# Performance work log

Measured on AMD Instinct MI355X. Metric: run time of the kernel, lower is better.

Reference implementation:

```python
import jax, jax.numpy as jnp
import numpy as np

B, S, D, H = 2, 2048, 2048, 16
HD = D // H
DFF = 4 * D
EPS = 1e-5


def _gelu(x):
    # tanh-approximate GELU as in the torch module
    c = jnp.sqrt(jnp.asarray(2.0 / jnp.pi, dtype=x.dtype))
    return 0.5 * x * (1.0 + jnp.tanh(c * (x + 0.044715 * x ** 3)))


def _layernorm(x, scale, shift):
    mean = jnp.mean(x, axis=-1, keepdims=True)
    var = jnp.mean((x - mean) ** 2, axis=-1, keepdims=True)  # unbiased=False
    return scale * (x - mean) / jnp.sqrt(var + EPS) + shift


def setup_inputs() -> dict:
    key = jax.random.key(0)
    ks = jax.random.split(key, 8)
    std = 0.02
    return {
        "x": jax.random.normal(ks[0], (B, S, D), dtype=jnp.float32),
        "Wq": std * jax.random.normal(ks[1], (D, D), dtype=jnp.float32),
        "Wk": std * jax.random.normal(ks[2], (D, D), dtype=jnp.float32),
        "Wv": std * jax.random.normal(ks[3], (D, D), dtype=jnp.float32),
        "Wo": std * jax.random.normal(ks[4], (D, D), dtype=jnp.float32),
        "bo": jnp.zeros((D,), dtype=jnp.float32),
        "ln1_scale": jnp.ones((D,), dtype=jnp.float32),
        "ln1_shift": jnp.zeros((D,), dtype=jnp.float32),
        "ln2_scale": jnp.ones((D,), dtype=jnp.float32),
        "ln2_shift": jnp.zeros((D,), dtype=jnp.float32),
        "W1": std * jax.random.normal(ks[5], (D, DFF), dtype=jnp.float32),
        "b1": jnp.zeros((DFF,), dtype=jnp.float32),
        "W2": std * jax.random.normal(ks[6], (DFF, D), dtype=jnp.float32),
        "b2": jnp.zeros((D,), dtype=jnp.float32),
    }


def _attention(x, Wq, Wk, Wv, Wo, bo):
    b, s, d = x.shape
    q = (x @ Wq).reshape(b, s, H, HD).transpose(0, 2, 1, 3)  # bhsd
    k = (x @ Wk).reshape(b, s, H, HD).transpose(0, 2, 1, 3)
    v = (x @ Wv).reshape(b, s, H, HD).transpose(0, 2, 1, 3)
    scores = jnp.einsum("bhqd,bhkd->bhqk", q, k)
    causal = jnp.tril(jnp.ones((s, s), dtype=bool))
    scores = jnp.where(causal, scores, -jnp.inf)
    w = jax.nn.softmax(scores / jnp.sqrt(jnp.asarray(HD, dtype=x.dtype)), axis=-1)
    ctx = jnp.einsum("bhqk,bhkd->bhqd", w, v)
    ctx = ctx.transpose(0, 2, 1, 3).reshape(b, s, d)
    return ctx @ Wo + bo


def reference(x, Wq, Wk, Wv, Wo, bo, ln1_scale, ln1_shift, ln2_scale, ln2_shift, W1, b1, W2, b2):
    # pre-LN transformer block; dropout rate 0 -> identity
    h = x + _attention(_layernorm(x, ln1_scale, ln1_shift), Wq, Wk, Wv, Wo, bo)
    y = _gelu(_layernorm(h, ln2_scale, ln2_shift) @ W1 + b1)
    return h + (y @ W2 + b2)
```

## Files before the change

### kernel.cpp

```cpp
#include <hip/hip_runtime.h>
#include <cmath>


typedef unsigned short u16;
typedef unsigned int   u32;
typedef float  f32x4   __attribute__((ext_vector_type(4)));
typedef short  s16x8   __attribute__((ext_vector_type(8)));
typedef short  s16x4   __attribute__((ext_vector_type(4)));
typedef __bf16 bf16x8  __attribute__((ext_vector_type(8)));

#define DEV __device__ __forceinline__

DEV u16 f2bf(float f) {
  union { float f; u32 u; } v; v.f = f;
  u32 u = v.u;
  u += 0x7fffu + ((u >> 16) & 1u);
  return (u16)(u >> 16);
}

DEV f32x4 mfma16(s16x8 a, s16x8 b, f32x4 c) {
  return __builtin_amdgcn_mfma_f32_16x16x32_bf16(
      __builtin_bit_cast(bf16x8, a), __builtin_bit_cast(bf16x8, b), c, 0, 0, 0);
}

DEV float gelu_f(float x) {
  const float c = 0.7978845608028654f;
  const float z = c * (x + 0.044715f * x * x * x);
  const float e = __expf(2.0f * z);
  const float th = 1.0f - 2.0f / (e + 1.0f);
  return 0.5f * x * (1.0f + th);
}

DEV void gload16(const u16* g, u16* l) {
  __builtin_amdgcn_global_load_lds(
      (const __attribute__((address_space(1))) u32*)(const void*)g,
      (__attribute__((address_space(3))) u32*)(void*)l, 16, 0, 0);
}

__global__ __launch_bounds__(256) void transpose_cast(
    const float* __restrict__ W, u16* __restrict__ Wt, int K, int N) {
  __shared__ float tile[32][33];
  const int n0 = blockIdx.x * 32, k0 = blockIdx.y * 32;
  const int tx = threadIdx.x, ty = threadIdx.y;
#pragma unroll
  for (int i = 0; i < 4; ++i)
    tile[ty + 8 * i][tx] = W[(size_t)(k0 + ty + 8 * i) * N + n0 + tx];
  __syncthreads();
#pragma unroll
  for (int i = 0; i < 4; ++i)
    Wt[(size_t)(n0 + ty + 8 * i) * K + k0 + tx] = f2bf(tile[tx][ty + 8 * i]);
}

__global__ __launch_bounds__(256) void transpose_v(
    const u16* __restrict__ QKV, u16* __restrict__ VT) {
  __shared__ u16 tile[32][33];
  const int s0 = blockIdx.x * 32;
  const int d0 = blockIdx.y * 32;
  const int bh = blockIdx.z;
  const int b = bh >> 4, h = bh & 15;
  const int tx = threadIdx.x, ty = threadIdx.y;
  const u16* src = QKV + (long)b * 2048 * 6144 + 4096 + h * 128;
#pragma unroll
  for (int i = 0; i < 4; ++i)
    tile[ty + 8 * i][tx] = src[(long)(s0 + ty + 8 * i) * 6144 + d0 + tx];
  __syncthreads();
  u16* dst = VT + (long)bh * 128 * 2048;
#pragma unroll
  for (int i = 0; i < 4; ++i)
    dst[(long)(d0 + ty + 8 * i) * 2048 + s0 + tx] = tile[tx][ty + 8 * i];
}

__global__ __launch_bounds__(256) void ln_kernel(
    const float* __restrict__ X, const float* __restrict__ sc,
    const float* __restrict__ sh, u16* __restrict__ Y) {
  const int row = blockIdx.x, t = threadIdx.x;
  const float* xr = X + (size_t)row * 2048;
  float4 v0 = ((const float4*)xr)[t];
  float4 v1 = ((const float4*)xr)[t + 256];
  float s  = v0.x + v0.y + v0.z + v0.w + v1.x + v1.y + v1.z + v1.w;
  float qs = v0.x*v0.x + v0.y*v0.y + v0.z*v0.z + v0.w*v0.w
           + v1.x*v1.x + v1.y*v1.y + v1.z*v1.z + v1.w*v1.w;
#pragma unroll
  for (int off = 1; off < 64; off <<= 1) {
    s  += __shfl_xor(s, off);
    qs += __shfl_xor(qs, off);
  }
  __shared__ float rs[4], rq[4];
  if ((t & 63) == 0) { rs[t >> 6] = s; rq[t >> 6] = qs; }
  __syncthreads();
  const float st = rs[0] + rs[1] + rs[2] + rs[3];
  const float qt = rq[0] + rq[1] + rq[2] + rq[3];
  const float mean = st * (1.0f / 2048.0f);
  const float var  = qt * (1.0f / 2048.0f) - mean * mean;
  const float rstd = rsqrtf(var + 1e-5f);

  u16* yr = Y + (size_t)row * 2048;
  const int c0 = t * 4, c1 = 1024 + t * 4;
  s16x4 o0, o1;
  o0[0] = (short)f2bf(sc[c0+0] * (v0.x - mean) * rstd + sh[c0+0]);
  o0[1] = (short)f2bf(sc[c0+1] * (v0.y - mean) * rstd + sh[c0+1]);
  o0[2] = (short)f2bf(sc[c0+2] * (v0.z - mean) * rstd + sh[c0+2]);
  o0[3] = (short)f2bf(sc[c0+3] * (v0.w - mean) * rstd + sh[c0+3]);
  o1[0] = (short)f2bf(sc[c1+0] * (v1.x - mean) * rstd + sh[c1+0]);
  o1[1] = (short)f2bf(sc[c1+1] * (v1.y - mean) * rstd + sh[c1+1]);
  o1[2] = (short)f2bf(sc[c1+2] * (v1.z - mean) * rstd + sh[c1+2]);
  o1[3] = (short)f2bf(sc[c1+3] * (v1.w - mean) * rstd + sh[c1+3]);
  *(s16x4*)(yr + c0) = o0;
  *(s16x4*)(yr + c1) = o1;
}

template<int MHALF, int STORE_BF16, int BIAS, int RES, int GELU_ACT>
__global__ __launch_bounds__(512, 2) void gemm8(
    const u16* __restrict__ A, const u16* __restrict__ Bt,
    const float* __restrict__ bias, const float* __restrict__ res,
    float* __restrict__ Cf, u16* __restrict__ Cb,
    int M, int N, int K, int rr, int rc) {
  constexpr int NPH   = 2 * MHALF;
  constexpr int ABUFS = (MHALF == 2) ? 2 : 3;
  constexpr int ASZ   = 8192 * MHALF;
  constexpr int BOFF  = ABUFS * ASZ;
  __shared__ u16 lds[BOFF + 2 * 16384];

  const int t9 = threadIdx.x;
  const int l = t9 & 63, w = t9 >> 6;
  const int r16 = l & 15, quad = l >> 4;
  const int wm = w >> 2, wn = w & 3;

  const int nbx = N >> 8;
  const int bid = blockIdx.x;
  const int xcd = bid & 7, j = bid >> 3;
  const int nregc = nbx / rc;
  const int m_t = (xcd / nregc) * rr + (j % rr);
  const int n_t = (xcd % nregc) * rc + (j / rr);
  const long m0 = (long)m_t * (128 * MHALF);
  const long n0 = (long)n_t * 256;

  const int NT = K >> 6;
  const int srow = t9 >> 3;
  const int scol = (t9 & 7) ^ (srow & 7);

  const u16* Abase = A  + (m0 + srow) * (long)K + scol * 8;
  const u16* Bbase = Bt + (n0 + srow) * (long)K + scol * 8;
  const long rowK64  = 64 * (long)K;
  const long rowK128 = 128 * (long)K;

  #define STAGE_A(tile, h) { \
    u16* d = &lds[((tile) % ABUFS) * ASZ + (h) * 8192 + w * 512]; \
    const u16* s = Abase + (h) * rowK128 + (long)(tile) * 64; \
    gload16(s, d); gload16(s + rowK64, d + 4096); }
  #define STAGE_B(tile, h) { \
    u16* d = &lds[BOFF + ((tile) & 1) * 16384 + (h) * 8192 + w * 512]; \
    const u16* s = Bbase + (h) * rowK128 + (long)(tile) * 64; \
    gload16(s, d); gload16(s + rowK64, d + 4096); }

  f32x4 acc[4 * MHALF][4] = {};

  if (MHALF == 2) {
    STAGE_B(0, 0); STAGE_B(0, 1); STAGE_A(0, 0); STAGE_A(0, 1);
    STAGE_B(1, 0); STAGE_B(1, 1);
    asm volatile("s_waitcnt vmcnt(4)" ::: "memory");
  } else {
    STAGE_B(0, 0); STAGE_B(0, 1); STAGE_A(0, 0); STAGE_A(1, 0);
    STAGE_B(1, 0); STAGE_B(1, 1);
    asm volatile("s_waitcnt vmcnt(6)" ::: "memory");
  }
  __builtin_amdgcn_sched_barrier(0);
  __builtin_amdgcn_s_barrier();

  s16x8 bf_[4][2];
  for (int t = 0; t < NT; ++t) {
    const int ab = t % ABUFS;
    const u16* Abuf = &lds[ab * ASZ];
    const u16* Bbuf = &lds[BOFF + (t & 1) * 16384];
#pragma unroll
    for (int p = 0; p < NPH; ++p) {
      if (p == 0) {
#pragma unroll
        for (int ni = 0; ni < 4; ++ni) {
          const int brow = wn * 64 + ni * 16 + r16;
#pragma unroll
          for (int ks = 0; ks < 2; ++ks)
            bf_[ni][ks] = *(const s16x8*)&Bbuf[brow * 64 + ((ks * 4 + quad) ^ (brow & 7)) * 8];
        }
      }
      s16x8 af[2][2];
#pragma unroll
      for (int mi = 0; mi < 2; ++mi) {
        const int arow = (MHALF == 2 ? wm * 128 : wm * 64) + (2 * p + mi) * 16 + r16;
#pragma unroll
        for (int ks = 0; ks < 2; ++ks)
          af[mi][ks] = *(const s16x8*)&Abuf[arow * 64 + ((ks * 4 + quad) ^ (arow & 7)) * 8];
      }
      if (MHALF == 2) {
        if (p < 2)       { if (t + 1 < NT) STAGE_A(t + 1, p); }
        else             { if (t + 2 < NT) STAGE_B(t + 2, p - 2); }
      } else {
        if (p == 0)      { if (t + 2 < NT) STAGE_A(t + 2, 0); }
        else             { if (t + 2 < NT) { STAGE_B(t + 2, 0); STAGE_B(t + 2, 1); } }
      }
      __builtin_amdgcn_sched_barrier(0);
      __builtin_amdgcn_s_barrier();
      asm volatile("s_waitcnt lgkmcnt(0)" ::: "memory");
      __builtin_amdgcn_sched_barrier(0);
      __builtin_amdgcn_s_setprio(1);
#pragma unroll
      for (int mi = 0; mi < 2; ++mi)
#pragma unroll
        for (int ni = 0; ni < 4; ++ni)
#pragma unroll
          for (int ks = 0; ks < 2; ++ks)
            acc[2 * p + mi][ni] = mfma16(af[mi][ks], bf_[ni][ks], acc[2 * p + mi][ni]);
      __builtin_amdgcn_s_setprio(0);
      __builtin_amdgcn_sched_barrier(0);
      if (p == NPH - 1) {
        if (MHALF == 2) {
          if (t + 2 < NT) { asm volatile("s_waitcnt vmcnt(4)" ::: "memory"); }
          else            { asm volatile("s_waitcnt vmcnt(0)" ::: "memory"); }
        } else {
          if (t + 2 < NT) { asm volatile("s_waitcnt vmcnt(6)" ::: "memory"); }
          else            { asm volatile("s_waitcnt vmcnt(0)" ::: "memory"); }
        }
        __builtin_amdgcn_sched_barrier(0);
      }
      __builtin_amdgcn_s_barrier();
    }
  }
  #undef STAGE_A
  #undef STAGE_B

#pragma unroll
  for (int mi = 0; mi < 4 * MHALF; ++mi) {
#pragma unroll
    for (int ni = 0; ni < 4; ++ni) {
#pragma unroll
      for (int r = 0; r < 4; ++r) {
        const long gr = m0 + (MHALF == 2 ? wm * 128 : wm * 64) + mi * 16 + quad * 4 + r;
        const long gc = n0 + wn * 64 + ni * 16 + r16;
        float v = acc[mi][ni][r];
        if (BIAS)     v += bias[gc];
        if (GELU_ACT) v  = gelu_f(v);
        if (RES)      v += res[gr * N + gc];
        if (STORE_BF16) Cb[gr * N + gc] = f2bf(v);
        else            Cf[gr * N + gc] = v;
      }
    }
  }
}

__global__ __launch_bounds__(256) void attn_kernel(
    const u16* __restrict__ QKV, const u16* __restrict__ VT,
    u16* __restrict__ CTX) {
  __shared__ u16 Ks[2][64 * 128];
  __shared__ u16 Vs[2][128 * 64];
  __shared__ u16 Pl[4][16 * 64];

  const int t = threadIdx.x;
  const int lane = t & 63, w = t >> 6;
  const int r16 = lane & 15, quad = lane >> 4;
  const int h = blockIdx.y, b = blockIdx.z;
  const long LDQ = 6144;
  const u16* Qb = QKV + (long)b * 2048 * LDQ + h * 128;
  const u16* Kb = Qb + 2048;
  const u16* Vtb = VT + (long)(b * 16 + h) * 128 * 2048;
  u16* Pw = Pl[w];
  const float scale = 0.08838834764831845f;

  const int k_row = t >> 4;
  const int k_slot = t & 15;
  const int v_row = t >> 3;
  const int v_slot = t & 7;

#define STAGE_KV(kt_, buf_)                                                    \
  {                                                                            \
    const int kb_ = (kt_) * 64;                                                \
    _Pragma("unroll") for (int i = 0; i < 4; ++i) {                            \
      const int row = i * 16 + k_row;                                          \
      gload16(Kb + (long)(kb_ + row) * LDQ + (k_slot ^ (row & 7)) * 8,         \
              &Ks[buf_][i * 2048 + w * 512]);                                  \
    }                                                                          \
    _Pragma("unroll") for (int i = 0; i < 4; ++i) {                            \
      const int d_ = i * 32 + v_row;                                           \
      gload16(Vtb + (long)d_ * 2048 + kb_ + (v_slot ^ (d_ & 7)) * 8,           \
              &Vs[buf_][i * 2048 + w * 512]);                                  \
    }                                                                          \
  }

  for (int half = 0; half < 2; ++half) {
    const int qt = half ? (31 - (int)blockIdx.x) : (int)blockIdx.x;
    const int qw = qt * 64 + w * 16;

    s16x8 aq[4];
#pragma unroll
    for (int ks = 0; ks < 4; ++ks)
      aq[ks] = *(const s16x8*)(Qb + (long)(qw + r16) * LDQ + ks * 32 + quad * 8);

    f32x4 o[8] = {};
    float mrun[4], lrun[4];
#pragma unroll
    for (int r = 0; r < 4; ++r) { mrun[r] = -1e30f; lrun[r] = 0.0f; }

    __builtin_amdgcn_s_barrier();
    STAGE_KV(0, 0);
    asm volatile("s_waitcnt vmcnt(0)" ::: "memory");
    __builtin_amdgcn_s_barrier();

    for (int kt = 0; kt <= qt; ++kt) {
      const int kbase = kt * 64;
      const int cur = kt & 1;
      if (kt < qt) STAGE_KV(kt + 1, cur ^ 1);

      if (kbase <= qw + 15) {
        f32x4 sc[4];
#pragma unroll
        for (int kh = 0; kh < 4; ++kh) {
          f32x4 z = {};
          sc[kh] = z;
          const int krow = kh * 16 + r16;
#pragma unroll
          for (int ks = 0; ks < 4; ++ks) {
            const s16x8 bk =
                *(const s16x8*)&Ks[cur][krow * 128 + ((ks * 4 + quad) ^ (krow & 7)) * 8];
            sc[kh] = mfma16(aq[ks], bk, sc[kh]);
          }
        }
        const bool need_mask = (kbase + 63 > qw);
        float alpha[4];
#pragma unroll
        for (int r = 0; r < 4; ++r) {
          const int q = qw + quad * 4 + r;
          float sv[4];
#pragma unroll
          for (int kh = 0; kh < 4; ++kh) {
            float s = sc[kh][r] * scale;
            if (need_mask && (kbase + kh * 16 + r16 > q)) s = -1e30f;
            sv[kh] = s;
          }
          float mx = fmaxf(fmaxf(sv[0], sv[1]), fmaxf(sv[2], sv[3]));
#pragma unroll
          for (int off = 1; off < 16; off <<= 1) mx = fmaxf(mx, __shfl_xor(mx, off));
          const float mn = fmaxf(mrun[r], mx);
          alpha[r] = __expf(mrun[r] - mn);
          mrun[r] = mn;
          const int prow = quad * 4 + r;
          float ps = 0.0f;
#pragma unroll
          for (int kh = 0; kh < 4; ++kh) {
            const float p = __expf(sv[kh] - mn);
            ps += p;
            Pw[(prow * 64 + kh * 16 + r16) ^ ((prow & 7) << 3)] = f2bf(p);
          }
          lrun[r] = lrun[r] * alpha[r] + ps;
        }
        if (alpha[0] != 1.0f || alpha[1] != 1.0f || alpha[2] != 1.0f || alpha[3] != 1.0f) {
#pragma unroll
          for (int ds = 0; ds < 8; ++ds)
#pragma unroll
            for (int r = 0; r < 4; ++r) o[ds][r] *= alpha[r];
        }
#pragma unroll
        for (int s = 0; s < 2; ++s) {
          const s16x8 ap =
              *(const s16x8*)&Pw[(r16 * 64 + s * 32 + quad * 8) ^ ((r16 & 7) << 3)];
#pragma unroll
          for (int ds = 0; ds < 8; ++ds) {
            const int d = ds * 16 + r16;
            const s16x8 bv =
                *(const s16x8*)&Vs[cur][d * 64 + ((s * 4 + quad) ^ (d & 7)) * 8];
            o[ds] = mfma16(ap, bv, o[ds]);
          }
        }
      }

      asm volatile("s_waitcnt vmcnt(0)" ::: "memory");
      __builtin_amdgcn_s_barrier();
    }

#pragma unroll
    for (int r = 0; r < 4; ++r)
#pragma unroll
      for (int off = 1; off < 16; off <<= 1) lrun[r] += __shfl_xor(lrun[r], off);

#pragma unroll
    for (int ds = 0; ds < 8; ++ds)
#pragma unroll
      for (int r = 0; r < 4; ++r) {
        const float v = o[ds][r] / lrun[r];
        CTX[(long)(b * 2048 + qw + quad * 4 + r) * 2048 + h * 128 + ds * 16 + r16] = f2bf(v);
      }
  }
#undef STAGE_KV
}

extern "C" void kernel_launch(void* const* d_in, const int* in_sizes, int n_in,
                              void* d_out, int out_size, void* d_ws, size_t ws_size,
                              hipStream_t stream) {
  (void)in_sizes; (void)n_in; (void)out_size; (void)ws_size;
  const float* x    = (const float*)d_in[0];
  const float* Wq   = (const float*)d_in[1];
  const float* Wk   = (const float*)d_in[2];
  const float* Wv   = (const float*)d_in[3];
  const float* Wo   = (const float*)d_in[4];
  const float* bo   = (const float*)d_in[5];
  const float* ln1s = (const float*)d_in[6];
  const float* ln1b = (const float*)d_in[7];
  const float* ln2s = (const float*)d_in[8];
  const float* ln2b = (const float*)d_in[9];
  const float* W1   = (const float*)d_in[10];
  const float* b1   = (const float*)d_in[11];
  const float* W2   = (const float*)d_in[12];
  const float* b2   = (const float*)d_in[13];
  float* out = (float*)d_out;

  const int Mtok = 4096, D = 2048, DFF = 8192, NQKV = 6144;

  char* w = (char*)d_ws;
  u16* Wt_qkv = (u16*)w;  w += (size_t)NQKV * D * 2;
  u16* Wt_o   = (u16*)w;  w += (size_t)D * D * 2;
  u16* Wt_1   = (u16*)w;  w += (size_t)DFF * D * 2;
  u16* Wt_2   = (u16*)w;  w += (size_t)D * DFF * 2;
  u16* Xln    = (u16*)w;  w += (size_t)Mtok * D * 2;
  u16* QKV    = (u16*)w;  w += (size_t)Mtok * NQKV * 2;
  u16* CTX    = (u16*)w;  w += (size_t)Mtok * D * 2;
  u16* Y1     = QKV;
  u16* VTb    = Wt_qkv;
  float* Hbuf = (float*)w; w += (size_t)Mtok * D * 4;

  const dim3 tb(32, 8, 1);
  transpose_cast<<<dim3(D / 32, D / 32), tb, 0, stream>>>(Wq, Wt_qkv,                    D, D);
  transpose_cast<<<dim3(D / 32, D / 32), tb, 0, stream>>>(Wk, Wt_qkv + (size_t)D * D,    D, D);
  transpose_cast<<<dim3(D / 32, D / 32), tb, 0, stream>>>(Wv, Wt_qkv + (size_t)2 * D * D,D, D);
  transpose_cast<<<dim3(D / 32, D / 32), tb, 0, stream>>>(Wo, Wt_o,                      D, D);
  transpose_cast<<<dim3(DFF / 32, D / 32), tb, 0, stream>>>(W1, Wt_1,                    D, DFF);
  transpose_cast<<<dim3(D / 32, DFF / 32), tb, 0, stream>>>(W2, Wt_2,                    DFF, D);

  ln_kernel<<<Mtok, 256, 0, stream>>>(x, ln1s, ln1b, Xln);

  gemm8<1, 1, 0, 0, 0><<<dim3(768), 512, 0, stream>>>(
      Xln, Wt_qkv, nullptr, nullptr, nullptr, QKV, Mtok, NQKV, D, 16, 6);

  transpose_v<<<dim3(64, 4, 32), tb, 0, stream>>>(QKV, VTb);

  attn_kernel<<<dim3(16, 16, 2), 256, 0, stream>>>(QKV, VTb, CTX);

  gemm8<1, 0, 1, 1, 0><<<dim3(256), 512, 0, stream>>>(
      CTX, Wt_o, bo, x, Hbuf, nullptr, Mtok, D, D, 8, 4);

  ln_kernel<<<Mtok, 256, 0, stream>>>(Hbuf, ln2s, ln2b, Xln);

  gemm8<2, 1, 1, 0, 1><<<dim3(512), 512, 0, stream>>>(
      Xln, Wt_1, b1, nullptr, nullptr, Y1, Mtok, DFF, D, 8, 8);

  gemm8<1, 0, 1, 1, 0><<<dim3(256), 512, 0, stream>>>(
      Y1, Wt_2, b2, Hbuf, out, nullptr, Mtok, D, DFF, 8, 4);
}
```

Baseline: 625.7 us.

## Add phased 256x256 GEMM kernel with interleaved prefetch for FFN up-projection

Adds a new gemm256 kernel for the W1 GEMM (bias+GELU, bf16 output). It splits each K-tile into four LDS-read/MFMA phases, issues next-tile global loads between them, and uses explicit waitcnt, barriers and setprio so memory traffic overlaps compute. It also sets launch bounds to 2 blocks per CU. The goal is to hide load latency and cut stalls in the largest GEMM, at the cost of hand-tuned wait counts that are fragile.

```diff
diff --git a/kernel.cpp b/kernel.cpp
--- a/kernel.cpp
+++ b/kernel.cpp
@@ -240,6 +240,150 @@
         if (BIAS)     v += bias[gc];
         if (GELU_ACT) v  = gelu_f(v);
         if (RES)      v += res[gr * N + gc];
+        if (STORE_BF16) Cb[gr * N + gc] = f2bf(v);
+        else            Cf[gr * N + gc] = v;
+      }
+    }
+  }
+}
+
+template<int STORE_BF16, int BIAS, int GELU_ACT>
+__global__ __launch_bounds__(512, 2) void gemm256(
+    const u16* __restrict__ A, const u16* __restrict__ Bt,
+    const float* __restrict__ bias,
+    float* __restrict__ Cf, u16* __restrict__ Cb,
+    int M, int N, int K, int rr, int rc) {
+  __shared__ u16 ldsA[2 * 16384];
+  __shared__ u16 ldsB[2 * 16384];
+
+  const int t9 = threadIdx.x;
+  const int l = t9 & 63, w = t9 >> 6;
+  const int r16 = l & 15, quad = l >> 4;
+  const int wm = w >> 2, wn = w & 3;
+
+  const int nbx = N >> 8;
+  const int bid = blockIdx.x;
+  const int xcd = bid & 7, j = bid >> 3;
+  const int nregc = nbx / rc;
+  const int m_t = (xcd / nregc) * rr + (j % rr);
+  const int n_t = (xcd % nregc) * rc + (j / rr);
+  const long m0 = (long)m_t * 256;
+  const long n0 = (long)n_t * 256;
+
+  const int NT = K >> 6;
+  const int srow = t9 >> 3;
+  const int scol = (t9 & 7) ^ (srow & 7);
+
+  const u16* Abase = A  + (m0 + srow) * (long)K + scol * 8;
+  const u16* Bbase = Bt + (n0 + srow) * (long)K + scol * 8;
+  const long rowK64 = 64 * (long)K;
+
+  #define SA(tile, q) gload16(Abase + (q) * rowK64 + (long)(tile) * 64, \
+                              &ldsA[((tile) & 1) * 16384 + (q) * 4096 + w * 512])
+  #define SB(tile, q) gload16(Bbase + (q) * rowK64 + (long)(tile) * 64, \
+                              &ldsB[((tile) & 1) * 16384 + (q) * 4096 + w * 512])
+
+  #define DSREAD_PHASE(mh, nh) { \
+    _Pragma("unroll") for (int ni = 0; ni < 2; ++ni) { \
+      const int br = wn * 64 + ((nh) * 2 + ni) * 16 + r16; \
+      _Pragma("unroll") for (int ks = 0; ks < 2; ++ks) \
+        bf[ni][ks] = *(const s16x8*)&Bbuf[br * 64 + ((ks * 4 + quad) ^ (br & 7)) * 8]; } \
+    _Pragma("unroll") for (int mi = 0; mi < 4; ++mi) { \
+      const int ar = wm * 128 + ((mh) * 4 + mi) * 16 + r16; \
+      _Pragma("unroll") for (int ks = 0; ks < 2; ++ks) \
+        af[mi][ks] = *(const s16x8*)&Abuf[ar * 64 + ((ks * 4 + quad) ^ (ar & 7)) * 8]; } }
+
+  #define MFMA_PHASE(mh, nh) \
+    _Pragma("unroll") for (int ks = 0; ks < 2; ++ks) \
+    _Pragma("unroll") for (int mi = 0; mi < 4; ++mi) \
+    _Pragma("unroll") for (int ni = 0; ni < 2; ++ni) \
+      acc[(mh) * 4 + mi][(nh) * 2 + ni] = \
+        mfma16(af[mi][ks], bf[ni][ks], acc[(mh) * 4 + mi][(nh) * 2 + ni]);
+
+  #define PH_MID \
+    asm volatile("s_waitcnt lgkmcnt(8)" ::: "memory"); \
+    __builtin_amdgcn_sched_barrier(0); \
+    __builtin_amdgcn_s_barrier(); \
+    asm volatile("s_waitcnt lgkmcnt(0)" ::: "memory"); \
+    __builtin_amdgcn_sched_barrier(0); \
+    __builtin_amdgcn_s_setprio(1);
+  #define PH_TAIL \
+    __builtin_amdgcn_s_setprio(0); \
+    __builtin_amdgcn_sched_barrier(0);
+
+  f32x4 acc[8][4] = {};
+
+  SB(0, 0); SB(0, 1); SB(0, 2); SB(0, 3);
+  SA(0, 0); SA(0, 2);
+  SA(0, 1); SA(0, 3);
+  if (NT > 1) {
+    SA(1, 0); SA(1, 2);
+    asm volatile("s_waitcnt vmcnt(4)" ::: "memory");
+  } else {
+    asm volatile("s_waitcnt vmcnt(2)" ::: "memory");
+  }
+  __builtin_amdgcn_sched_barrier(0);
+  __builtin_amdgcn_s_barrier();
+
+  for (int t = 0; t < NT; ++t) {
+    const u16* Abuf = &ldsA[(t & 1) * 16384];
+    const u16* Bbuf = &ldsB[(t & 1) * 16384];
+    const bool p1n = (t + 1 < NT);
+    const bool p2n = (t + 2 < NT);
+    s16x8 af[4][2], bf[2][2];
+
+    DSREAD_PHASE(0, 0);
+    if (p1n) { SB(t + 1, 0); SB(t + 1, 1); }
+    PH_MID
+    MFMA_PHASE(0, 0);
+    PH_TAIL
+    __builtin_amdgcn_s_barrier();
+
+    DSREAD_PHASE(0, 1);
+    if (p1n) { SB(t + 1, 2); SB(t + 1, 3); }
+    PH_MID
+    MFMA_PHASE(0, 1);
+    PH_TAIL
+    if (p1n) { asm volatile("s_waitcnt vmcnt(6)" ::: "memory"); }
+    else     { asm volatile("s_waitcnt vmcnt(0)" ::: "memory"); }
+    __builtin_amdgcn_sched_barrier(0);
+    __builtin_amdgcn_s_barrier();
+
+    DSREAD_PHASE(1, 0);
+    if (p2n) { SA(t + 2, 0); SA(t + 2, 2); }
+    PH_MID
+    MFMA_PHASE(1, 0);
+    PH_TAIL
+    __builtin_amdgcn_s_barrier();
+
+    DSREAD_PHASE(1, 1);
+    if (p1n) { SA(t + 1, 1); SA(t + 1, 3); }
+    PH_MID
+    MFMA_PHASE(1, 1);
+    PH_TAIL
+    if (p2n)      { asm volatile("s_waitcnt vmcnt(4)" ::: "memory"); }
+    else if (p1n) { asm volatile("s_waitcnt vmcnt(2)" ::: "memory"); }
+    __builtin_amdgcn_sched_barrier(0);
+    __builtin_amdgcn_s_barrier();
+  }
+  #undef SA
+  #undef SB
+  #undef DSREAD_PHASE
+  #undef MFMA_PHASE
+  #undef PH_MID
+  #undef PH_TAIL
+
+#pragma unroll
+  for (int mi = 0; mi < 8; ++mi) {
+#pragma unroll
+    for (int ni = 0; ni < 4; ++ni) {
+#pragma unroll
+      for (int r = 0; r < 4; ++r) {
+        const long gr = m0 + wm * 128 + mi * 16 + quad * 4 + r;
+        const long gc = n0 + wn * 64 + ni * 16 + r16;
+        float v = acc[mi][ni][r];
+        if (BIAS)     v += bias[gc];
+        if (GELU_ACT) v  = gelu_f(v);
         if (STORE_BF16) Cb[gr * N + gc] = f2bf(v);
         else            Cf[gr * N + gc] = v;
       }
@@ -447,8 +591,8 @@
 
   ln_kernel<<<Mtok, 256, 0, stream>>>(Hbuf, ln2s, ln2b, Xln);
 
-  gemm8<2, 1, 1, 0, 1><<<dim3(512), 512, 0, stream>>>(
-      Xln, Wt_1, b1, nullptr, nullptr, Y1, Mtok, DFF, D, 8, 8);
+  gemm256<1, 1, 1><<<dim3(512), 512, 0, stream>>>(
+      Xln, Wt_1, b1, nullptr, Y1, Mtok, DFF, D, 8, 8);
 
   gemm8<1, 0, 1, 1, 0><<<dim3(256), 512, 0, stream>>>(
       Y1, Wt_2, b2, Hbuf, out, nullptr, Mtok, D, DFF, 8, 4);
```

Result: slower. 669.1 us (+6.9%).
